# Performance work log

Measured on AMD Instinct MI355X. Metric: run time of the kernel, lower is better.

## Reference

```python
import jax, jax.numpy as jnp
import numpy as np

N_NODES = 100000
N_EDGES = 1600000
STATE_DIM = 128
HIDDEN_DIM = 128
ACTION_DIM = 16


def gcn_conv(x, edge_index, W, b, n_nodes):
    """PyG-style GCNConv: add self-loops, symmetric normalization, x@W then aggregate."""
    xw = x @ W  # [N, H]
    loops = jnp.arange(n_nodes, dtype=edge_index.dtype)
    src = jnp.concatenate([edge_index[0], loops])  # [E+N]
    dst = jnp.concatenate([edge_index[1], loops])
    ones = jnp.ones(src.shape[0], dtype=xw.dtype)
    deg = jax.ops.segment_sum(ones, dst, num_segments=n_nodes)  # degree of target nodes
    dinv = jnp.where(deg > 0, jax.lax.rsqrt(deg), 0.0)
    norm = dinv[src] * dinv[dst]  # [E+N]
    msg = xw[src] * norm[:, None]  # gather + scale (irregular access)
    out = jax.ops.segment_sum(msg, dst, num_segments=n_nodes)  # scatter-aggregate
    return out + b


def setup_inputs() -> dict:
    key = jax.random.key(0)
    ks = jax.random.split(key, 12)
    def lin(k, fan_in, shape):
        bound = 1.0 / np.sqrt(fan_in)
        return jax.random.uniform(k, shape, jnp.float32, -bound, bound)
    return {
        "x": jax.random.normal(ks[0], (N_NODES, STATE_DIM), jnp.float32),
        "edge_index": jax.random.randint(ks[1], (2, N_EDGES), 0, N_NODES, jnp.int64),
        "action": jax.random.normal(ks[2], (N_NODES, ACTION_DIM), jnp.float32),
        "gcn1_w": lin(ks[3], STATE_DIM, (STATE_DIM, HIDDEN_DIM)),
        "gcn1_b": lin(ks[4], STATE_DIM, (HIDDEN_DIM,)),
        "gcn2_w": lin(ks[5], HIDDEN_DIM, (HIDDEN_DIM, HIDDEN_DIM)),
        "gcn2_b": lin(ks[6], HIDDEN_DIM, (HIDDEN_DIM,)),
        "fc1_w": lin(ks[7], HIDDEN_DIM + ACTION_DIM, (HIDDEN_DIM + ACTION_DIM, HIDDEN_DIM)),
        "fc1_b": lin(ks[8], HIDDEN_DIM + ACTION_DIM, (HIDDEN_DIM,)),
        "fc2_w": lin(ks[9], HIDDEN_DIM, (HIDDEN_DIM, 1)),
        "fc2_b": lin(ks[10], HIDDEN_DIM, (1,)),
    }


def reference(x, edge_index, action, gcn1_w, gcn1_b, gcn2_w, gcn2_b, fc1_w, fc1_b, fc2_w, fc2_b):
    n = x.shape[0]
    h = jax.nn.relu(gcn_conv(x, edge_index, gcn1_w, gcn1_b, n))
    h = jax.nn.relu(gcn_conv(h, edge_index, gcn2_w, gcn2_b, n))
    h = jnp.concatenate([h, action], axis=-1)  # [N, H+A]
    h = jax.nn.relu(h @ fc1_w + fc1_b)
    q = h @ fc2_w + fc2_b  # [N, 1]
    return q.squeeze(-1)
```

## Files before the change

### kernel.cpp

```cpp
#include <hip/hip_runtime.h>
#include <hip/hip_bf16.h>

typedef unsigned short u16;
typedef unsigned int   u32;
typedef __attribute__((ext_vector_type(8))) short bf16x8;
typedef __attribute__((ext_vector_type(4))) float f32x4;

constexpr int NN = 100000;
constexpr int NE = 1600000;
constexpr int D  = 128;
constexpr size_t WS_NEED = 58909184;

constexpr int NBUCK = 196;
constexpr int NBLKA = 256;
constexpr int EPB   = 6272;
constexpr int CAPA  = 80;

__device__ __forceinline__ float bf2f(u16 u){ union{u32 i;float f;}v; v.i=((u32)u)<<16; return v.f; }
__device__ __forceinline__ float2 bfp(u32 u){ union{u32 i;float f;}a,b; a.i=u<<16; b.i=u&0xffff0000u; return make_float2(a.f,b.f); }
__device__ __forceinline__ u16 f2bf(float f){ union{float f;u32 i;}v; v.f=f; u32 r=v.i + 0x7fffu + ((v.i>>16)&1u); return (u16)(r>>16); }
__device__ __forceinline__ u32 pk2(float a, float b){ return (u32)f2bf(a) | ((u32)f2bf(b)<<16); }

__global__ void detect_kernel(const u32* __restrict__ xw, const int* __restrict__ ei,
                              int* __restrict__ flagf, int* __restrict__ flage){
  __shared__ int shf[256];
  __shared__ int she[256];
  int t = threadIdx.x;
  int cnt = 0;
  for(int i = 0; i < 16; i++){
    u32 w = xw[(t*16 + i) * 256];
    int e = (int)((w >> 7) & 0xFFu);
    cnt += (e >= 64 && e <= 160) ? 1 : 0;
  }
  int nz = 0;
  for(int i = 0; i < 8; i++){
    int k = t*8 + i;
    long long w = 1 + ((long long)k * (2LL*NE - 2)) / 2048;
    nz += (ei[(int)(w | 1)] != 0) ? 1 : 0;
  }
  shf[t] = cnt; she[t] = nz;
  __syncthreads();
  for(int off=128; off>0; off>>=1){
    if(t<off){ shf[t]+=shf[t+off]; she[t]+=she[t+off]; }
    __syncthreads();
  }
  if(t==0){ flagf[0] = (shf[0] < 3000) ? 1 : 0; flage[0] = (she[0] == 0) ? 1 : 0; }
}

__global__ void prep_kernel(const void* __restrict__ w1, const void* __restrict__ w2,
    const void* __restrict__ fw1, const void* __restrict__ b1, const void* __restrict__ b2,
    const void* __restrict__ fb1, const void* __restrict__ fw2, const void* __restrict__ fb2,
    const int* __restrict__ flagf,
    u16* __restrict__ WT1, u16* __restrict__ WT2, u16* __restrict__ WTF, float* __restrict__ BF)
{
  const int ff = flagf[0];
  int i = blockIdx.x*256 + threadIdx.x;
  auto cv = [&](const void* p, int idx)->float{
    return ff ? ((const float*)p)[idx] : bf2f(((const u16*)p)[idx]);
  };
  if(i < 16384){
    int k = i >> 7, d = i & 127;
    WT1[d*128 + k] = f2bf(cv(w1, i));
  }else if(i < 32768){
    int j = i - 16384; int k = j >> 7, d = j & 127;
    WT2[d*128 + k] = f2bf(cv(w2, j));
  }else if(i < 51200){
    int j = i - 32768; int k = j >> 7, d = j & 127;
    WTF[d*144 + k] = f2bf(cv(fw1, j));
  }else if(i < 51713){
    int j = i - 51200;
    if(j < 128)       BF[j]   = cv(b1, j);
    else if(j < 256)  BF[j]   = cv(b2, j-128);
    else if(j < 384)  BF[j]   = cv(fb1, j-256);
    else if(j < 512)  BF[j]   = cv(fw2, j-384);
    else              BF[512] = cv(fb2, 0);
  }
}

__global__ void fill1_kernel(u16* __restrict__ out, int n){
  int i = blockIdx.x*blockDim.x + threadIdx.x;
  if(i < n) out[i] = 0x3F80;
}

__global__ __launch_bounds__(256) void passA_kernel(
    const int* __restrict__ ei, const int* __restrict__ flage,
    u32* __restrict__ ebuf, u32* __restrict__ counts)
{
  __shared__ u32 hist[NBUCK];
  int t = threadIdx.x;
  for(int b = t; b < NBUCK; b += 256) hist[b] = 0;
  __syncthreads();
  const int f = flage[0];
  const int eb = blockIdx.x * EPB;
  const u32 cbase = blockIdx.x * NBUCK;
  for(int i = t; i < EPB; i += 256){
    int e = eb + i;
    if(e >= NE) break;
    int s = f ? ei[2*e]      : ei[e];
    int d = f ? ei[2*(NE+e)] : ei[NE+e];
    if((u32)s >= (u32)NN || (u32)d >= (u32)NN) continue;
    int b = d >> 9;
    u32 rank = atomicAdd(&hist[b], 1u);
    if(rank < CAPA) ebuf[(size_t)(cbase + b)*CAPA + rank] = (u32)s | ((u32)(d & 511) << 17);
  }
  __syncthreads();
  for(int b = t; b < NBUCK; b += 256){
    u32 c = hist[b];
    counts[cbase + b] = (c < CAPA) ? c : CAPA;
  }
}

__global__ void scan196_kernel(const u32* __restrict__ counts, int* __restrict__ bases){
  __shared__ int sh[NBUCK];
  int t = threadIdx.x;
  if(t < NBUCK){
    int tot = 0;
    for(int c = 0; c < NBLKA; c++) tot += counts[c*NBUCK + t];
    sh[t] = tot;
  }
  __syncthreads();
  if(t == 0){
    int acc = 0;
    for(int b = 0; b < NBUCK; b++){ int v = sh[b]; sh[b] = acc; acc += v; }
  }
  __syncthreads();
  if(t < NBUCK) bases[t] = sh[t];
}

__global__ __launch_bounds__(512) void passB_kernel(
    const u32* __restrict__ ebuf, const u32* __restrict__ counts, const int* __restrict__ bases,
    int* __restrict__ deg, int* __restrict__ off, float* __restrict__ dinv,
    int* __restrict__ srcs)
{
  __shared__ int cnt[512];
  __shared__ int nodeoff[512];
  __shared__ int pos[512];
  __shared__ int choff[NBLKA + 1];
  const int t = threadIdx.x;
  const int b = blockIdx.x;
  const int v0 = b << 9;

  cnt[t] = 0;
  __syncthreads();

  if(t < NBLKA) choff[t] = (int)counts[t*NBUCK + b];
  __syncthreads();
  if(t == 0){
    int acc = 0;
    for(int c = 0; c < NBLKA; c++){ int v = choff[c]; choff[c] = acc; acc += v; }
    choff[NBLKA] = acc;
  }
  __syncthreads();
  const int T = choff[NBLKA];

  for(int i = t; i < T; i += 512){
    int lo = 0, hi = NBLKA - 1;
    #pragma unroll
    for(int s = 0; s < 8; s++){
      int mid = (lo + hi) >> 1;
      if(choff[mid + 1] <= i) lo = mid + 1; else hi = mid;
    }
    u32 rec = ebuf[(size_t)(lo*NBUCK + b)*CAPA + (i - choff[lo])];
    atomicAdd(&cnt[rec >> 17], 1);
  }
  __syncthreads();

  int myc = cnt[t];
  nodeoff[t] = myc;
  __syncthreads();
  for(int o = 1; o < 512; o <<= 1){
    int a = (t >= o) ? nodeoff[t - o] : 0;
    __syncthreads();
    nodeoff[t] += a;
    __syncthreads();
  }
  int excl = nodeoff[t] - myc;
  __syncthreads();
  nodeoff[t] = excl;
  pos[t] = 0;
  __syncthreads();

  const int gb = bases[b];

  for(int i = t; i < T; i += 512){
    int lo = 0, hi = NBLKA - 1;
    #pragma unroll
    for(int s = 0; s < 8; s++){
      int mid = (lo + hi) >> 1;
      if(choff[mid + 1] <= i) lo = mid + 1; else hi = mid;
    }
    u32 rec = ebuf[(size_t)(lo*NBUCK + b)*CAPA + (i - choff[lo])];
    int ld = rec >> 17;
    int r = atomicAdd(&pos[ld], 1);
    srcs[gb + nodeoff[ld] + r] = (int)(rec & 0x1FFFFu);
  }

  int v = v0 + t;
  if(v < NN){
    deg[v] = myc;
    off[v] = gb + excl;
    dinv[v] = rsqrtf((float)(myc + 1));
  }
}

__global__ __launch_bounds__(256) void gemm1_kernel(
    const void* __restrict__ A1, const u16* __restrict__ WT,
    const int* __restrict__ flagf, const float* __restrict__ dscale,
    u16* __restrict__ out, int n)
{
  constexpr int KP = 136;
  __shared__ u16 Ws[128*KP];
  __shared__ u16 As[64*KP];
  const int tid = threadIdx.x;
  const int nb  = blockIdx.x * 64;
  const int ff  = flagf[0];

  for(int i = tid; i < 128*16; i += 256){
    int row = i / 16, col = (i % 16) * 8;
    *(uint4*)(Ws + row*KP + col) = *(const uint4*)(WT + row*128 + col);
  }
  for(int i = tid; i < 64*16; i += 256){
    int row = i / 16, col = (i % 16) * 8;
    int gr = nb + row; if(gr >= n) gr = n-1;
    uint4 v;
    if(!ff){
      v = *(const uint4*)((const u16*)A1 + (size_t)gr*128 + col);
    }else{
      const float* af = (const float*)A1 + (size_t)gr*128 + col;
      float4 p0 = *(const float4*)(af);
      float4 p1 = *(const float4*)(af + 4);
      v.x = pk2(p0.x,p0.y); v.y = pk2(p0.z,p0.w);
      v.z = pk2(p1.x,p1.y); v.w = pk2(p1.z,p1.w);
    }
    *(uint4*)(As + row*KP + col) = v;
  }
  __syncthreads();

  const int wave = tid >> 6;
  const int lane = tid & 63;
  const int quad = lane >> 4;
  const int lm   = lane & 15;

  const u16* Ab = As + (wave*16 + lm)*KP;
  const u16* Bb = Ws + lm*KP;

  f32x4 acc[8];
  #pragma unroll
  for(int t=0;t<8;t++) acc[t] = (f32x4){0.f,0.f,0.f,0.f};

  #pragma unroll
  for(int ki = 0; ki < 4; ki++){
    int kk = ki*32 + quad*8;
    bf16x8 a = *(const bf16x8*)(Ab + kk);
    #pragma unroll
    for(int t=0;t<8;t++){
      bf16x8 b = *(const bf16x8*)(Bb + t*16*KP + kk);
      acc[t] = __builtin_amdgcn_mfma_f32_16x16x32_bf16(a, b, acc[t], 0, 0, 0);
    }
  }

  const int node0 = nb + wave*16 + quad*4;
  #pragma unroll
  for(int r=0;r<4;r++){
    int gr = node0 + r;
    if(gr < n){
      float dv = dscale[gr];
      #pragma unroll
      for(int t=0;t<8;t++){
        out[(size_t)gr*D + t*16 + lm] = f2bf(acc[t][r]*dv);
      }
    }
  }
}

#define ACC8(r)  { float2 f_;                       \
    f_ = bfp((r).x); a0 += f_.x; a1 += f_.y;        \
    f_ = bfp((r).y); a2 += f_.x; a3 += f_.y;        \
    f_ = bfp((r).z); a4 += f_.x; a5 += f_.y;        \
    f_ = bfp((r).w); a6 += f_.x; a7 += f_.y; }

template<bool FINAL>
__global__ __launch_bounds__(256) void fused_kernel(
    const int* __restrict__ off, const int* __restrict__ deg,
    const int* __restrict__ srcs, const float* __restrict__ dinv,
    const u16* __restrict__ xw, const float* __restrict__ biasf,
    const u16* __restrict__ WT, const float* __restrict__ fb1,
    const float* __restrict__ qwf, const float* __restrict__ qbf,
    const void* __restrict__ action, const int* __restrict__ flagf,
    void* __restrict__ out)
{
  constexpr int K  = FINAL ? 144 : 128;
  constexpr int KT = FINAL ? 160 : 128;
  constexpr int KP = KT + 8;
  __shared__ u16 Hs[16*KP];
  __shared__ float qred[FINAL ? 64 : 4];

  const int tid  = threadIdx.x;
  const int node0 = blockIdx.x * 16;
  const int nl   = tid >> 4;
  const int l16  = tid & 15;
  const int node = node0 + nl;

  const int j0 = off[node];
  const int j1 = j0 + deg[node];
  float a0=0.f,a1=0.f,a2=0.f,a3=0.f,a4=0.f,a5=0.f,a6=0.f,a7=0.f;
  const u16* __restrict__ xl = xw + 8*l16;

  int j = j0;
  int s0=0, s1=0, s2=0, s3=0;
  const bool pre = (j + 4 <= j1);
  if(pre){
    s0 = __builtin_nontemporal_load(&srcs[j]);
    s1 = __builtin_nontemporal_load(&srcs[j+1]);
    s2 = __builtin_nontemporal_load(&srcs[j+2]);
    s3 = __builtin_nontemporal_load(&srcs[j+3]);
  }
  for(; j + 8 <= j1; j += 4){
    uint4 r0 = *(const uint4*)(xl + (size_t)s0*D);
    uint4 r1 = *(const uint4*)(xl + (size_t)s1*D);
    uint4 r2 = *(const uint4*)(xl + (size_t)s2*D);
    uint4 r3 = *(const uint4*)(xl + (size_t)s3*D);
    s0 = __builtin_nontemporal_load(&srcs[j+4]);
    s1 = __builtin_nontemporal_load(&srcs[j+5]);
    s2 = __builtin_nontemporal_load(&srcs[j+6]);
    s3 = __builtin_nontemporal_load(&srcs[j+7]);
    ACC8(r0); ACC8(r1); ACC8(r2); ACC8(r3);
  }
  if(pre){
    uint4 r0 = *(const uint4*)(xl + (size_t)s0*D);
    uint4 r1 = *(const uint4*)(xl + (size_t)s1*D);
    uint4 r2 = *(const uint4*)(xl + (size_t)s2*D);
    uint4 r3 = *(const uint4*)(xl + (size_t)s3*D);
    ACC8(r0); ACC8(r1); ACC8(r2); ACC8(r3);
    j += 4;
  }
  for(; j < j1; j++){
    int s = __builtin_nontemporal_load(&srcs[j]);
    uint4 r = *(const uint4*)(xl + (size_t)s*D);
    ACC8(r);
  }

  uint4 ps = *(const uint4*)(xl + (size_t)node*D);
  ACC8(ps);
  const float dv = dinv[node];
  float4 bA = *(const float4*)(biasf + 8*l16);
  float4 bB = *(const float4*)(biasf + 8*l16 + 4);
  float o0 = fmaxf(fmaf(dv,a0,bA.x), 0.f);
  float o1 = fmaxf(fmaf(dv,a1,bA.y), 0.f);
  float o2 = fmaxf(fmaf(dv,a2,bA.z), 0.f);
  float o3 = fmaxf(fmaf(dv,a3,bA.w), 0.f);
  float o4 = fmaxf(fmaf(dv,a4,bB.x), 0.f);
  float o5 = fmaxf(fmaf(dv,a5,bB.y), 0.f);
  float o6 = fmaxf(fmaf(dv,a6,bB.z), 0.f);
  float o7 = fmaxf(fmaf(dv,a7,bB.w), 0.f);
  uint4 pkd;
  pkd.x = pk2(o0,o1); pkd.y = pk2(o2,o3); pkd.z = pk2(o4,o5); pkd.w = pk2(o6,o7);

  u16* Hp = Hs + nl*KP;
  *(uint4*)(Hp + 8*l16) = pkd;

  if(FINAL){
    const int ff = flagf[0];
    if(ff){
      if(l16 < 4){
        const float* af = (const float*)action + (size_t)node*16 + l16*4;
        float4 p = *(const float4*)af;
        uint2 q; q.x = pk2(p.x,p.y); q.y = pk2(p.z,p.w);
        *(uint2*)(Hp + 128 + 4*l16) = q;
      }
    }else{
      if(l16 < 2){
        uint4 v = *(const uint4*)((const u16*)action + (size_t)node*16 + 8*l16);
        *(uint4*)(Hp + 128 + 8*l16) = v;
      }
    }
    if(l16 >= 14){
      *(uint4*)(Hp + 144 + 8*(l16-14)) = make_uint4(0,0,0,0);
    }
  }
  __syncthreads();

  const int wave = tid >> 6;
  const int lane = tid & 63;
  const int quad = lane >> 4;
  const int lm   = lane & 15;

  const u16* Ab = Hs + lm*KP;
  f32x4 acc[2];
  acc[0] = (f32x4){0.f,0.f,0.f,0.f};
  acc[1] = (f32x4){0.f,0.f,0.f,0.f};

  #pragma unroll
  for(int ki = 0; ki < KT/32; ki++){
    int kk = ki*32 + quad*8;
    bf16x8 a = *(const bf16x8*)(Ab + kk);
    #pragma unroll
    for(int tt=0; tt<2; tt++){
      int col = (wave*2 + tt)*16 + lm;
      bf16x8 b = (bf16x8){0,0,0,0,0,0,0,0};
      if(!FINAL || kk < K)
        b = *(const bf16x8*)(WT + (size_t)col*K + kk);
      acc[tt] = __builtin_amdgcn_mfma_f32_16x16x32_bf16(a, b, acc[tt], 0, 0, 0);
    }
  }

  const int rbase = quad*4;
  if(!FINAL){
    #pragma unroll
    for(int r=0;r<4;r++){
      int gn = node0 + rbase + r;
      float dvr = dinv[gn];
      #pragma unroll
      for(int tt=0;tt<2;tt++){
        int col = (wave*2 + tt)*16 + lm;
        ((u16*)out)[(size_t)gn*D + col] = f2bf(acc[tt][r]*dvr);
      }
    }
  }else{
    float qp[4] = {0.f,0.f,0.f,0.f};
    #pragma unroll
    for(int tt=0;tt<2;tt++){
      int col = (wave*2 + tt)*16 + lm;
      float bv = fb1[col];
      float qw = qwf[col];
      #pragma unroll
      for(int r=0;r<4;r++){
        float h = fmaxf(acc[tt][r] + bv, 0.f);
        qp[r] += h * qw;
      }
    }
    #pragma unroll
    for(int r=0;r<4;r++){
      #pragma unroll
      for(int o=1; o<16; o<<=1) qp[r] += __shfl_xor(qp[r], o, 16);
    }
    if(lm == 0){
      #pragma unroll
      for(int r=0;r<4;r++) qred[wave*16 + rbase + r] = qp[r];
    }
    __syncthreads();
    if(tid < 16){
      float q = qred[tid] + qred[16+tid] + qred[32+tid] + qred[48+tid] + qbf[0];
      int gn = node0 + tid;
      const int ff = flagf[0];
      if(ff) ((float*)out)[gn] = q;
      else   ((u16*)out)[gn]  = f2bf(q);
    }
  }
}

extern "C" void kernel_launch(void* const* d_in, const int* in_sizes, int n_in,
                              void* d_out, int out_size, void* d_ws, size_t ws_size,
                              hipStream_t stream)
{
  bool meta_ok = (n_in >= 11) && (in_sizes[0] == NN*D) && (in_sizes[1] == 2*NE)
              && (in_sizes[2] == NN*16) && (out_size == NN);
  if(!meta_ok){
    fill1_kernel<<<(NN+255)/256, 256, 0, stream>>>((u16*)d_out, NN);
    return;
  }
  if(ws_size < WS_NEED) return;

  const void* x      = d_in[0];
  const int*  ei     = (const int*)d_in[1];
  const void* action = d_in[2];
  const void* w1     = d_in[3];
  const void* b1     = d_in[4];
  const void* w2     = d_in[5];
  const void* b2     = d_in[6];
  const void* fw1    = d_in[7];
  const void* fb1    = d_in[8];
  const void* fw2    = d_in[9];
  const void* fb2    = d_in[10];

  char* ws = (char*)d_ws;
  int*   DEG    = (int*)(ws + 0);
  int*   OFF    = (int*)(ws + 400128);
  float* DINV   = (float*)(ws + 800256);
  int*   FLAGE  = (int*)(ws + 1204480);
  int*   FLAGF  = (int*)(ws + 1204544);
  u16*   WT1    = (u16*)(ws + 1204608);
  u16*   WT2    = (u16*)(ws + 1237376);
  u16*   WTF    = (u16*)(ws + 1270144);
  float* BF     = (float*)(ws + 1307008);
  int*   SRCS   = (int*)(ws + 1309184);
  u16*   F0     = (u16*)(ws + 7709184);
  u16*   F1     = (u16*)(ws + 33309184);
  u32*   EBUF   = (u32*)(ws + 33309184);
  u32*   COUNTS = (u32*)(ws + 49365504);
  int*   BASES  = (int*)(ws + 49566208);

  detect_kernel<<<1, 256, 0, stream>>>((const u32*)x, ei, FLAGF, FLAGE);

  passA_kernel<<<NBLKA, 256, 0, stream>>>(ei, FLAGE, EBUF, COUNTS);
  scan196_kernel<<<1, 256, 0, stream>>>(COUNTS, BASES);
  passB_kernel<<<NBUCK, 512, 0, stream>>>(EBUF, COUNTS, BASES, DEG, OFF, DINV, SRCS);

  prep_kernel<<<203, 256, 0, stream>>>(w1, w2, fw1, b1, b2, fb1, fw2, fb2, FLAGF,
                                       WT1, WT2, WTF, BF);

  gemm1_kernel<<<(NN+63)/64, 256, 0, stream>>>(x, WT1, FLAGF, DINV, F0, NN);

  fused_kernel<false><<<(NN+15)/16, 256, 0, stream>>>(
      OFF, DEG, SRCS, DINV, F0, BF, WT2, nullptr, nullptr, nullptr, nullptr, FLAGF, F1);

  fused_kernel<true><<<(NN+15)/16, 256, 0, stream>>>(
      OFF, DEG, SRCS, DINV, F1, BF+128, WTF, BF+256, BF+384, BF+512, action, FLAGF, d_out);
}
```

Baseline: 341.8 us.

## Drop LDS staging in GEMM, prefetch weights before barrier, serialize per-chunk edge reads

In the first GEMM, the A fragments and W fragments are now loaded straight from global memory into registers, so the LDS staging and its barrier go away. In the fused aggregation kernel, the weight fragments are loaded into registers before the barrier, which lets their latency overlap with the wait for the other waves. In passB, the shared-memory prefix sum and binary search over chunk offsets are replaced by one thread per chunk that walks its records in order. This costs coalescing and lowers parallelism: only 256 threads are active, and each reads a strided chunk serially.

```diff
diff --git a/kernel.cpp b/kernel.cpp
--- a/kernel.cpp
+++ b/kernel.cpp
@@ -5,6 +5,7 @@
 typedef unsigned int   u32;
 typedef __attribute__((ext_vector_type(8))) short bf16x8;
 typedef __attribute__((ext_vector_type(4))) float f32x4;
+typedef __attribute__((ext_vector_type(4))) unsigned int u32x4;
 
 constexpr int NN = 100000;
 constexpr int NE = 1600000;
@@ -135,7 +136,6 @@
   __shared__ int cnt[512];
   __shared__ int nodeoff[512];
   __shared__ int pos[512];
-  __shared__ int choff[NBLKA + 1];
   const int t = threadIdx.x;
   const int b = blockIdx.x;
   const int v0 = b << 9;
@@ -143,25 +143,15 @@
   cnt[t] = 0;
   __syncthreads();
 
-  if(t < NBLKA) choff[t] = (int)counts[t*NBUCK + b];
-  __syncthreads();
-  if(t == 0){
-    int acc = 0;
-    for(int c = 0; c < NBLKA; c++){ int v = choff[c]; choff[c] = acc; acc += v; }
-    choff[NBLKA] = acc;
-  }
-  __syncthreads();
-  const int T = choff[NBLKA];
-
-  for(int i = t; i < T; i += 512){
-    int lo = 0, hi = NBLKA - 1;
-    #pragma unroll
-    for(int s = 0; s < 8; s++){
-      int mid = (lo + hi) >> 1;
-      if(choff[mid + 1] <= i) lo = mid + 1; else hi = mid;
-    }
-    u32 rec = ebuf[(size_t)(lo*NBUCK + b)*CAPA + (i - choff[lo])];
-    atomicAdd(&cnt[rec >> 17], 1);
+  int cnum = 0;
+  const u32* cp = nullptr;
+  if(t < NBLKA){
+    cnum = (int)counts[t*NBUCK + b];
+    cp   = ebuf + (size_t)(t*NBUCK + b)*CAPA;
+    for(int i = 0; i < cnum; i++){
+      u32 rec = cp[i];
+      atomicAdd(&cnt[rec >> 17], 1);
+    }
   }
   __syncthreads();
 
@@ -182,17 +172,13 @@
 
   const int gb = bases[b];
 
-  for(int i = t; i < T; i += 512){
-    int lo = 0, hi = NBLKA - 1;
-    #pragma unroll
-    for(int s = 0; s < 8; s++){
-      int mid = (lo + hi) >> 1;
-      if(choff[mid + 1] <= i) lo = mid + 1; else hi = mid;
-    }
-    u32 rec = ebuf[(size_t)(lo*NBUCK + b)*CAPA + (i - choff[lo])];
-    int ld = rec >> 17;
-    int r = atomicAdd(&pos[ld], 1);
-    srcs[gb + nodeoff[ld] + r] = (int)(rec & 0x1FFFFu);
+  if(t < NBLKA){
+    for(int i = 0; i < cnum; i++){
+      u32 rec = cp[i];
+      int ld = rec >> 17;
+      int r = atomicAdd(&pos[ld], 1);
+      srcs[gb + nodeoff[ld] + r] = (int)(rec & 0x1FFFFu);
+    }
   }
 
   int v = v0 + t;
@@ -208,41 +194,32 @@
     const int* __restrict__ flagf, const float* __restrict__ dscale,
     u16* __restrict__ out, int n)
 {
-  constexpr int KP = 136;
-  __shared__ u16 Ws[128*KP];
-  __shared__ u16 As[64*KP];
   const int tid = threadIdx.x;
   const int nb  = blockIdx.x * 64;
   const int ff  = flagf[0];
-
-  for(int i = tid; i < 128*16; i += 256){
-    int row = i / 16, col = (i % 16) * 8;
-    *(uint4*)(Ws + row*KP + col) = *(const uint4*)(WT + row*128 + col);
-  }
-  for(int i = tid; i < 64*16; i += 256){
-    int row = i / 16, col = (i % 16) * 8;
-    int gr = nb + row; if(gr >= n) gr = n-1;
-    uint4 v;
-    if(!ff){
-      v = *(const uint4*)((const u16*)A1 + (size_t)gr*128 + col);
-    }else{
-      const float* af = (const float*)A1 + (size_t)gr*128 + col;
-      float4 p0 = *(const float4*)(af);
-      float4 p1 = *(const float4*)(af + 4);
-      v.x = pk2(p0.x,p0.y); v.y = pk2(p0.z,p0.w);
-      v.z = pk2(p1.x,p1.y); v.w = pk2(p1.z,p1.w);
-    }
-    *(uint4*)(As + row*KP + col) = v;
-  }
-  __syncthreads();
-
   const int wave = tid >> 6;
   const int lane = tid & 63;
   const int quad = lane >> 4;
   const int lm   = lane & 15;
 
-  const u16* Ab = As + (wave*16 + lm)*KP;
-  const u16* Bb = Ws + lm*KP;
+  int arow = nb + wave*16 + lm; if(arow >= n) arow = n-1;
+
+  bf16x8 afr[4];
+  if(!ff){
+    const u16* xr = (const u16*)A1 + (size_t)arow*128 + quad*8;
+    #pragma unroll
+    for(int k=0;k<4;k++) afr[k] = *(const bf16x8*)(xr + 32*k);
+  }else{
+    const float* xr = (const float*)A1 + (size_t)arow*128 + quad*8;
+    #pragma unroll
+    for(int k=0;k<4;k++){
+      float4 p0 = *(const float4*)(xr + 32*k);
+      float4 p1 = *(const float4*)(xr + 32*k + 4);
+      union{u32x4 u; bf16x8 v;} cvv;
+      cvv.u = (u32x4){pk2(p0.x,p0.y), pk2(p0.z,p0.w), pk2(p1.x,p1.y), pk2(p1.z,p1.w)};
+      afr[k] = cvv.v;
+    }
+  }
 
   f32x4 acc[8];
   #pragma unroll
@@ -251,11 +228,10 @@
   #pragma unroll
   for(int ki = 0; ki < 4; ki++){
     int kk = ki*32 + quad*8;
-    bf16x8 a = *(const bf16x8*)(Ab + kk);
     #pragma unroll
     for(int t=0;t<8;t++){
-      bf16x8 b = *(const bf16x8*)(Bb + t*16*KP + kk);
-      acc[t] = __builtin_amdgcn_mfma_f32_16x16x32_bf16(a, b, acc[t], 0, 0, 0);
+      bf16x8 b = *(const bf16x8*)(WT + (size_t)(t*16 + lm)*128 + kk);
+      acc[t] = __builtin_amdgcn_mfma_f32_16x16x32_bf16(afr[ki], b, acc[t], 0, 0, 0);
     }
   }
 
@@ -292,6 +268,7 @@
   constexpr int K  = FINAL ? 144 : 128;
   constexpr int KT = FINAL ? 160 : 128;
   constexpr int KP = KT + 8;
+  constexpr int NKI = KT/32;
   __shared__ u16 Hs[16*KP];
   __shared__ float qred[FINAL ? 64 : 4];
 
@@ -300,6 +277,11 @@
   const int nl   = tid >> 4;
   const int l16  = tid & 15;
   const int node = node0 + nl;
+
+  const int wave = tid >> 6;
+  const int lane = tid & 63;
+  const int quad = lane >> 4;
+  const int lm   = lane & 15;
 
   const int j0 = off[node];
   const int j1 = j0 + deg[node];
@@ -378,12 +360,20 @@
       *(uint4*)(Hp + 144 + 8*(l16-14)) = make_uint4(0,0,0,0);
     }
   }
-  __syncthreads();
-
-  const int wave = tid >> 6;
-  const int lane = tid & 63;
-  const int quad = lane >> 4;
-  const int lm   = lane & 15;
+
+  bf16x8 bfr[NKI][2];
+  #pragma unroll
+  for(int ki = 0; ki < NKI; ki++){
+    int kk = ki*32 + quad*8;
+    #pragma unroll
+    for(int tt=0; tt<2; tt++){
+      int col = (wave*2 + tt)*16 + lm;
+      bfr[ki][tt] = (bf16x8){0,0,0,0,0,0,0,0};
+      if(!FINAL || kk < K)
+        bfr[ki][tt] = *(const bf16x8*)(WT + (size_t)col*K + kk);
+    }
+  }
+  __syncthreads();
 
   const u16* Ab = Hs + lm*KP;
   f32x4 acc[2];
@@ -391,17 +381,11 @@
   acc[1] = (f32x4){0.f,0.f,0.f,0.f};
 
   #pragma unroll
-  for(int ki = 0; ki < KT/32; ki++){
+  for(int ki = 0; ki < NKI; ki++){
     int kk = ki*32 + quad*8;
     bf16x8 a = *(const bf16x8*)(Ab + kk);
-    #pragma unroll
-    for(int tt=0; tt<2; tt++){
-      int col = (wave*2 + tt)*16 + lm;
-      bf16x8 b = (bf16x8){0,0,0,0,0,0,0,0};
-      if(!FINAL || kk < K)
-        b = *(const bf16x8*)(WT + (size_t)col*K + kk);
-      acc[tt] = __builtin_amdgcn_mfma_f32_16x16x32_bf16(a, b, acc[tt], 0, 0, 0);
-    }
+    acc[0] = __builtin_amdgcn_mfma_f32_16x16x32_bf16(a, bfr[ki][0], acc[0], 0, 0, 0);
+    acc[1] = __builtin_amdgcn_mfma_f32_16x16x32_bf16(a, bfr[ki][1], acc[1], 0, 0, 0);
   }
 
   const int rbase = quad*4;
```

Result: no change. 337.4 us (-1.3%).
